# Kernel tuning notes

Hardware: AMD Instinct MI355X
Metric: run time of the kernel (lower is better)

## Reference

```python
import jax, jax.numpy as jnp
import numpy as np

N, X_DIM, Y_DIM, HID = 1024, 256, 256, 256  # HID = hidden_size // 2


def setup_inputs() -> dict:
    key = jax.random.key(0)
    ks = jax.random.split(key, 11)
    s_in = 1.0 / np.sqrt(X_DIM)
    s_h = 1.0 / np.sqrt(HID)
    return {
        "x_samples": jax.random.normal(ks[0], (N, X_DIM), jnp.float32),
        "y_samples": jax.random.normal(ks[1], (N, Y_DIM), jnp.float32),
        "z_samples": jax.random.normal(ks[2], (N, Y_DIM), jnp.float32),
        "w1_mu": jax.random.uniform(ks[3], (HID, X_DIM), jnp.float32, -s_in, s_in),
        "b1_mu": jax.random.uniform(ks[4], (HID,), jnp.float32, -s_in, s_in),
        "w2_mu": jax.random.uniform(ks[5], (Y_DIM, HID), jnp.float32, -s_h, s_h),
        "b2_mu": jax.random.uniform(ks[6], (Y_DIM,), jnp.float32, -s_h, s_h),
        "w1_lv": jax.random.uniform(ks[7], (HID, X_DIM), jnp.float32, -s_in, s_in),
        "b1_lv": jax.random.uniform(ks[8], (HID,), jnp.float32, -s_in, s_in),
        "w2_lv": jax.random.uniform(ks[9], (Y_DIM, HID), jnp.float32, -s_h, s_h),
        "b2_lv": jax.random.uniform(ks[10], (Y_DIM,), jnp.float32, -s_h, s_h),
    }


def reference(x_samples, y_samples, z_samples,
              w1_mu, b1_mu, w2_mu, b2_mu,
              w1_lv, b1_lv, w2_lv, b2_lv):
    # MLP heads (torch Linear: x @ W.T + b)
    h_mu = jax.nn.relu(x_samples @ w1_mu.T + b1_mu)
    mu = h_mu @ w2_mu.T + b2_mu                       # [N, D]
    h_lv = jax.nn.relu(x_samples @ w1_lv.T + b1_lv)
    logvar = jnp.tanh(h_lv @ w2_lv.T + b2_lv)          # [N, D]

    inv2var = 1.0 / (2.0 * jnp.exp(logvar))           # [N, D]

    # positive: per-sample conditional log-density term
    positive = -((mu - y_samples) ** 2 + (mu - z_samples) ** 2) * inv2var  # [N, D]

    # negative: mean over all pairings (i: prediction, j: sample)
    # pairwise squared diffs materialize [N, N, D] like the original broadcast
    pred = mu[:, None, :]                              # [N, 1, D]
    sq = (y_samples[None, :, :] - pred) ** 2 + (z_samples[None, :, :] - pred) ** 2
    negative = -sq.mean(axis=1) * inv2var              # [N, D]

    return jax.nn.relu(positive.sum(axis=-1) - negative.sum(axis=-1)).mean()
```

## Files before the change

### kernel.cpp

```cpp
#include <hip/hip_runtime.h>
#include <math.h>

constexpr int LSB = 72;

typedef short bf16x8 __attribute__((ext_vector_type(8)));
typedef float f32x4  __attribute__((ext_vector_type(4)));

__device__ __forceinline__ unsigned short f2bf_rne(float f) {
    unsigned u = __float_as_uint(f);
    unsigned r = (u + 0x7fff + ((u >> 16) & 1)) >> 16;
    return (unsigned short)r;
}
__device__ __forceinline__ float bf2f(unsigned short h) {
    return __uint_as_float(((unsigned)h) << 16);
}
__device__ __forceinline__ void split4(float4 v, ushort4& hi, ushort4& lo) {
    hi.x = f2bf_rne(v.x); lo.x = f2bf_rne(v.x - bf2f(hi.x));
    hi.y = f2bf_rne(v.y); lo.y = f2bf_rne(v.y - bf2f(hi.y));
    hi.z = f2bf_rne(v.z); lo.z = f2bf_rne(v.z - bf2f(hi.z));
    hi.w = f2bf_rne(v.w); lo.w = f2bf_rne(v.w - bf2f(hi.w));
}

__global__ __launch_bounds__(256, 2)
void k1_layer1(const float* __restrict__ x,
               const float* __restrict__ w1m, const float* __restrict__ w1l,
               const float* __restrict__ b1m, const float* __restrict__ b1l,
               const float* __restrict__ w2m, const float* __restrict__ w2l,
               unsigned short* __restrict__ hmH, unsigned short* __restrict__ hmL,
               unsigned short* __restrict__ hlH, unsigned short* __restrict__ hlL,
               unsigned short* __restrict__ w2mH, unsigned short* __restrict__ w2mL,
               unsigned short* __restrict__ w2lH, unsigned short* __restrict__ w2lL,
               const float* __restrict__ y, const float* __restrict__ z,
               float* __restrict__ pA1, float* __restrict__ pB1,
               float* __restrict__ rowAcc) {
    const int bid = blockIdx.x, t = threadIdx.x;
    const int head = bid & 1, ct = (bid >> 1) & 7, rt = bid >> 4;
    const int rowBase = rt * 32, colBase = ct * 32;
    const int w = t >> 6, lane = t & 63, quad = lane >> 4, mr = lane & 15;
    const int mt = w & 1, nt = w >> 1;

    const float* Bw   = head ? w1l : w1m;
    const float* bias = head ? b1l : b1m;
    unsigned short* CH = head ? hlH : hmH;
    unsigned short* CL = head ? hlL : hmL;

    __shared__ __align__(16) unsigned short Ah[32][LSB], Al[32][LSB];
    __shared__ __align__(16) unsigned short Bh[32][LSB], Bl[32][LSB];

    f32x4 acc = {0.f, 0.f, 0.f, 0.f};

    for (int kt = 0; kt < 256; kt += 64) {
#pragma unroll
        for (int p = 0; p < 2; p++) {
            int idx = p * 256 + t;
            int r = idx >> 4, k4 = idx & 15;
            float4 av = *(const float4*)&x[(rowBase + r) * 256 + kt + k4 * 4];
            float4 bv = *(const float4*)&Bw[(colBase + r) * 256 + kt + k4 * 4];
            ushort4 h4, l4;
            split4(av, h4, l4);
            *(ushort4*)&Ah[r][k4 * 4] = h4;
            *(ushort4*)&Al[r][k4 * 4] = l4;
            split4(bv, h4, l4);
            *(ushort4*)&Bh[r][k4 * 4] = h4;
            *(ushort4*)&Bl[r][k4 * 4] = l4;
        }
        __syncthreads();

#pragma unroll
        for (int kk = 0; kk < 64; kk += 32) {
            int ko = kk + quad * 8;
            bf16x8 ah = *(const bf16x8*)&Ah[mt * 16 + mr][ko];
            bf16x8 al = *(const bf16x8*)&Al[mt * 16 + mr][ko];
            bf16x8 bh = *(const bf16x8*)&Bh[nt * 16 + mr][ko];
            bf16x8 bl = *(const bf16x8*)&Bl[nt * 16 + mr][ko];
            acc = __builtin_amdgcn_mfma_f32_16x16x32_bf16(ah, bh, acc, 0, 0, 0);
            acc = __builtin_amdgcn_mfma_f32_16x16x32_bf16(ah, bl, acc, 0, 0, 0);
            acc = __builtin_amdgcn_mfma_f32_16x16x32_bf16(al, bh, acc, 0, 0, 0);
        }
        __syncthreads();
    }

    {
        int cg = colBase + nt * 16 + mr;
        float bb = bias[cg];
#pragma unroll
        for (int reg = 0; reg < 4; reg++) {
            int rg = rowBase + mt * 16 + quad * 4 + reg;
            float v = fmaxf(acc[reg] + bb, 0.f);
            unsigned short hi = f2bf_rne(v);
            CH[rg * 256 + cg] = hi;
            CL[rg * 256 + cg] = f2bf_rne(v - bf2f(hi));
        }
    }

    if (bid < 256) {
        int off = bid * 256 + t;
        float vm = w2m[off], vl = w2l[off];
        unsigned short h1 = f2bf_rne(vm);
        w2mH[off] = h1; w2mL[off] = f2bf_rne(vm - bf2f(h1));
        unsigned short h2 = f2bf_rne(vl);
        w2lH[off] = h2; w2lL[off] = f2bf_rne(vl - bf2f(h2));
    }

    if (bid < 256) {
        float sA = 0.f, sB = 0.f;
        int base = bid * 4 * 256 + t;
#pragma unroll
        for (int j = 0; j < 4; j++) {
            float yv = y[base + j * 256];
            float zv = z[base + j * 256];
            sA += yv * yv + zv * zv;
            sB += yv + zv;
        }
        pA1[bid * 256 + t] = sA;
        pB1[bid * 256 + t] = sB;
    }

    if (bid < 4) rowAcc[bid * 256 + t] = 0.f;
}

__global__ __launch_bounds__(256, 2)
void k2_fused(const unsigned short* __restrict__ hmH, const unsigned short* __restrict__ hmL,
              const unsigned short* __restrict__ hlH, const unsigned short* __restrict__ hlL,
              const unsigned short* __restrict__ w2mH, const unsigned short* __restrict__ w2mL,
              const unsigned short* __restrict__ w2lH, const unsigned short* __restrict__ w2lL,
              const float* __restrict__ b2m, const float* __restrict__ b2l,
              const float* __restrict__ y, const float* __restrict__ z,
              const float* __restrict__ pA1, const float* __restrict__ pB1,
              float* __restrict__ rowAcc) {
    const int bid = blockIdx.x, t = threadIdx.x;
    const int rt = bid >> 4, ct = bid & 15;
    const int rowBase = rt * 32, colBase = ct * 16;
    const int w = t >> 6, lane = t & 63, quad = lane >> 4, mr = lane & 15;
    const int h = w & 1, mt = w >> 1;

    __shared__ __align__(16) unsigned short Ast[2][2][32][LSB];
    __shared__ __align__(16) unsigned short Bst[2][2][16][LSB];
    __shared__ float Cx[2][32][17];
    __shared__ float part[16][16];
    __shared__ float mAf[16], mBf[16];

    const unsigned short* Aarr[4] = {hmH, hmL, hlH, hlL};
    const unsigned short* Barr[4] = {w2mH, w2mL, w2lH, w2lL};

    {
        int c = t & 15, g = t >> 4;
        int gc = colBase + c;
        float sA = 0.f, sB = 0.f;
        for (int j = 0; j < 16; j++) {
            int s = g * 16 + j;
            sA += pA1[s * 256 + gc];
        }
        part[g][c] = sA;
    }
    __syncthreads();
    if (t < 16) {
        float sA = 0.f;
#pragma unroll
        for (int g = 0; g < 16; g++) sA += part[g][t];
        mAf[t] = sA * (1.f / 1024.f);
    }
    __syncthreads();
    {
        int c = t & 15, g = t >> 4;
        int gc = colBase + c;
        float sB = 0.f;
        for (int j = 0; j < 16; j++) {
            int s = g * 16 + j;
            sB += pB1[s * 256 + gc];
        }
        part[g][c] = sB;
    }
    __syncthreads();
    if (t < 16) {
        float sB = 0.f;
#pragma unroll
        for (int g = 0; g < 16; g++) sB += part[g][t];
        mBf[t] = sB * (1.f / 1024.f);
    }

    f32x4 acc = {0.f, 0.f, 0.f, 0.f};

    for (int kt = 0; kt < 256; kt += 64) {
#pragma unroll
        for (int hp = 0; hp < 4; hp++) {
#pragma unroll
            for (int p = 0; p < 2; p++) {
                int idx = p * 256 + t;
                int r = idx >> 4, k4 = idx & 15;
                *(ushort4*)&Ast[hp >> 1][hp & 1][r][k4 * 4] =
                    *(const ushort4*)&Aarr[hp][(rowBase + r) * 256 + kt + k4 * 4];
            }
            {
                int r = t >> 4, k4 = t & 15;
                *(ushort4*)&Bst[hp >> 1][hp & 1][r][k4 * 4] =
                    *(const ushort4*)&Barr[hp][(colBase + r) * 256 + kt + k4 * 4];
            }
        }
        __syncthreads();

#pragma unroll
        for (int kk = 0; kk < 64; kk += 32) {
            int ko = kk + quad * 8;
            bf16x8 ah = *(const bf16x8*)&Ast[h][0][mt * 16 + mr][ko];
            bf16x8 al = *(const bf16x8*)&Ast[h][1][mt * 16 + mr][ko];
            bf16x8 bh = *(const bf16x8*)&Bst[h][0][mr][ko];
            bf16x8 bl = *(const bf16x8*)&Bst[h][1][mr][ko];
            acc = __builtin_amdgcn_mfma_f32_16x16x32_bf16(ah, bh, acc, 0, 0, 0);
            acc = __builtin_amdgcn_mfma_f32_16x16x32_bf16(ah, bl, acc, 0, 0, 0);
            acc = __builtin_amdgcn_mfma_f32_16x16x32_bf16(al, bh, acc, 0, 0, 0);
        }
        __syncthreads();
    }

    {
        const float* bias = h ? b2l : b2m;
        float bb = bias[colBase + mr];
#pragma unroll
        for (int reg = 0; reg < 4; reg++)
            Cx[h][mt * 16 + quad * 4 + reg][mr] = acc[reg] + bb;
    }
    __syncthreads();

    {
        int col = t & 15, rg = t >> 4;
        int gcol = colBase + col;
        float mA = mAf[col], mB = mBf[col];
#pragma unroll
        for (int rr = 0; rr < 2; rr++) {
            int row = rg * 2 + rr;
            int o = (rowBase + row) * 256 + gcol;
            float m  = Cx[0][row][col];
            float lv = tanhf(Cx[1][row][col]);
            float iv = 0.5f * expf(-lv);
            float yv = y[o];
            float zv = z[o];
            float Mt = mA - 2.f * m * mB + 2.f * m * m;
            float dy = m - yv, dz = m - zv;
            float term = iv * (Mt - dy * dy - dz * dz);
#pragma unroll
            for (int msk = 8; msk; msk >>= 1)
                term += __shfl_xor(term, msk, 16);
            if (col == 0) atomicAdd(&rowAcc[rowBase + row], term);
        }
    }
}

__global__ __launch_bounds__(256)
void k3_final(const float* __restrict__ rowAcc, float* __restrict__ out) {
    __shared__ float red[4];
    int t = threadIdx.x, lane = t & 63, wave = t >> 6;
    float v = 0.f;
#pragma unroll
    for (int p = 0; p < 4; p++)
        v += fmaxf(rowAcc[p * 256 + t], 0.f);
#pragma unroll
    for (int msk = 32; msk; msk >>= 1)
        v += __shfl_xor(v, msk, 64);
    if (lane == 0) red[wave] = v;
    __syncthreads();
    if (t == 0)
        out[0] = (red[0] + red[1] + red[2] + red[3]) * (1.f / 1024.f);
}

extern "C" void kernel_launch(void* const* d_in, const int* in_sizes, int n_in,
                              void* d_out, int out_size, void* d_ws, size_t ws_size,
                              hipStream_t stream) {
    const float* x   = (const float*)d_in[0];
    const float* y   = (const float*)d_in[1];
    const float* zs  = (const float*)d_in[2];
    const float* w1m = (const float*)d_in[3];
    const float* b1m = (const float*)d_in[4];
    const float* w2m = (const float*)d_in[5];
    const float* b2m = (const float*)d_in[6];
    const float* w1l = (const float*)d_in[7];
    const float* b1l = (const float*)d_in[8];
    const float* w2l = (const float*)d_in[9];
    const float* b2l = (const float*)d_in[10];
    float* out = (float*)d_out;

    char* ws = (char*)d_ws;
    float* pA1    = (float*)(ws);
    float* pB1    = (float*)(ws + (256u << 10));
    float* rowAcc = (float*)(ws + (512u << 10));
    unsigned short* hmH = (unsigned short*)(ws + (1024u << 10));
    unsigned short* hmL = (unsigned short*)(ws + (1536u << 10));
    unsigned short* hlH = (unsigned short*)(ws + (2048u << 10));
    unsigned short* hlL = (unsigned short*)(ws + (2560u << 10));
    unsigned short* w2mH = (unsigned short*)(ws + (3072u << 10));
    unsigned short* w2mL = (unsigned short*)(ws + (3200u << 10));
    unsigned short* w2lH = (unsigned short*)(ws + (3328u << 10));
    unsigned short* w2lL = (unsigned short*)(ws + (3456u << 10));

    k1_layer1<<<512, 256, 0, stream>>>(x, w1m, w1l, b1m, b1l, w2m, w2l,
                                       hmH, hmL, hlH, hlL,
                                       w2mH, w2mL, w2lH, w2lL,
                                       y, zs, pA1, pB1, rowAcc);
    k2_fused<<<512, 256, 0, stream>>>(hmH, hmL, hlH, hlL,
                                      w2mH, w2mL, w2lH, w2lL,
                                      b2m, b2l, y, zs, pA1, pB1, rowAcc);
    k3_final<<<1, 256, 0, stream>>>(rowAcc, out);
}
```

Measured before the change: 91.45 us.

## Split K across waves and double grid size in both GEMM kernels

Both GEMM kernels now use smaller output tiles (16 columns in layer 1, 16 rows in layer 2) with the K dimension split across wave pairs and partial sums reduced through shared memory, doubling block counts to 1040 and 1024. The y/z column-sum precompute moves to 16 dedicated blocks, each of which loops over 64 rows, and launch bounds rise to 4 blocks per CU. The aim is more parallelism and occupancy on a small problem, paid for with extra shared-memory reduction, more syncs, and redundant staging of x across more blocks.

```diff
diff --git a/kernel.cpp b/kernel.cpp
--- a/kernel.cpp
+++ b/kernel.cpp
@@ -21,7 +21,7 @@
     hi.w = f2bf_rne(v.w); lo.w = f2bf_rne(v.w - bf2f(hi.w));
 }
 
-__global__ __launch_bounds__(256, 2)
+__global__ __launch_bounds__(256, 4)
 void k1_layer1(const float* __restrict__ x,
                const float* __restrict__ w1m, const float* __restrict__ w1l,
                const float* __restrict__ b1m, const float* __restrict__ b1l,
@@ -34,45 +34,68 @@
                float* __restrict__ pA1, float* __restrict__ pB1,
                float* __restrict__ rowAcc) {
     const int bid = blockIdx.x, t = threadIdx.x;
-    const int head = bid & 1, ct = (bid >> 1) & 7, rt = bid >> 4;
-    const int rowBase = rt * 32, colBase = ct * 32;
+
+    if (bid < 16) {
+        float sA = 0.f, sB = 0.f;
+        int base = bid * 64 * 256 + t;
+        for (int j = 0; j < 64; j++) {
+            float yv = y[base + j * 256];
+            float zv = z[base + j * 256];
+            sA += yv * yv + zv * zv;
+            sB += yv + zv;
+        }
+        pA1[bid * 256 + t] = sA;
+        pB1[bid * 256 + t] = sB;
+        return;
+    }
+
+    const int g = bid - 16;
+    const int head = g & 1, ct = (g >> 1) & 15, rt = g >> 5;
+    const int rowBase = rt * 32, colBase = ct * 16;
     const int w = t >> 6, lane = t & 63, quad = lane >> 4, mr = lane & 15;
-    const int mt = w & 1, nt = w >> 1;
+    const int mt = w & 1, ks = w >> 1;
 
     const float* Bw   = head ? w1l : w1m;
     const float* bias = head ? b1l : b1m;
     unsigned short* CH = head ? hlH : hmH;
     unsigned short* CL = head ? hlL : hmL;
 
-    __shared__ __align__(16) unsigned short Ah[32][LSB], Al[32][LSB];
-    __shared__ __align__(16) unsigned short Bh[32][LSB], Bl[32][LSB];
+    __shared__ __align__(16) unsigned short Ast[2][2][32][LSB];
+    __shared__ __align__(16) unsigned short Bst[2][2][16][LSB];
+    __shared__ float Cx[2][16][17];
 
     f32x4 acc = {0.f, 0.f, 0.f, 0.f};
 
-    for (int kt = 0; kt < 256; kt += 64) {
+    for (int sub = 0; sub < 2; sub++) {
+#pragma unroll
+        for (int p = 0; p < 4; p++) {
+            int idx = p * 256 + t;
+            int q = idx >> 9, r = (idx >> 4) & 31, k4 = idx & 15;
+            float4 av = *(const float4*)&x[(rowBase + r) * 256 + q * 128 + sub * 64 + k4 * 4];
+            ushort4 h4, l4;
+            split4(av, h4, l4);
+            *(ushort4*)&Ast[q][0][r][k4 * 4] = h4;
+            *(ushort4*)&Ast[q][1][r][k4 * 4] = l4;
+        }
 #pragma unroll
         for (int p = 0; p < 2; p++) {
             int idx = p * 256 + t;
-            int r = idx >> 4, k4 = idx & 15;
-            float4 av = *(const float4*)&x[(rowBase + r) * 256 + kt + k4 * 4];
-            float4 bv = *(const float4*)&Bw[(colBase + r) * 256 + kt + k4 * 4];
+            int q = idx >> 8, r = (idx >> 4) & 15, k4 = idx & 15;
+            float4 bv = *(const float4*)&Bw[(colBase + r) * 256 + q * 128 + sub * 64 + k4 * 4];
             ushort4 h4, l4;
-            split4(av, h4, l4);
-            *(ushort4*)&Ah[r][k4 * 4] = h4;
-            *(ushort4*)&Al[r][k4 * 4] = l4;
             split4(bv, h4, l4);
-            *(ushort4*)&Bh[r][k4 * 4] = h4;
-            *(ushort4*)&Bl[r][k4 * 4] = l4;
+            *(ushort4*)&Bst[q][0][r][k4 * 4] = h4;
+            *(ushort4*)&Bst[q][1][r][k4 * 4] = l4;
         }
         __syncthreads();
 
 #pragma unroll
         for (int kk = 0; kk < 64; kk += 32) {
             int ko = kk + quad * 8;
-            bf16x8 ah = *(const bf16x8*)&Ah[mt * 16 + mr][ko];
-            bf16x8 al = *(const bf16x8*)&Al[mt * 16 + mr][ko];
-            bf16x8 bh = *(const bf16x8*)&Bh[nt * 16 + mr][ko];
-            bf16x8 bl = *(const bf16x8*)&Bl[nt * 16 + mr][ko];
+            bf16x8 ah = *(const bf16x8*)&Ast[ks][0][mt * 16 + mr][ko];
+            bf16x8 al = *(const bf16x8*)&Ast[ks][1][mt * 16 + mr][ko];
+            bf16x8 bh = *(const bf16x8*)&Bst[ks][0][mr][ko];
+            bf16x8 bl = *(const bf16x8*)&Bst[ks][1][mr][ko];
             acc = __builtin_amdgcn_mfma_f32_16x16x32_bf16(ah, bh, acc, 0, 0, 0);
             acc = __builtin_amdgcn_mfma_f32_16x16x32_bf16(ah, bl, acc, 0, 0, 0);
             acc = __builtin_amdgcn_mfma_f32_16x16x32_bf16(al, bh, acc, 0, 0, 0);
@@ -80,21 +103,27 @@
         __syncthreads();
     }
 
-    {
-        int cg = colBase + nt * 16 + mr;
+    if (ks == 1) {
+#pragma unroll
+        for (int reg = 0; reg < 4; reg++)
+            Cx[mt][quad * 4 + reg][mr] = acc[reg];
+    }
+    __syncthreads();
+    if (ks == 0) {
+        int cg = colBase + mr;
         float bb = bias[cg];
 #pragma unroll
         for (int reg = 0; reg < 4; reg++) {
             int rg = rowBase + mt * 16 + quad * 4 + reg;
-            float v = fmaxf(acc[reg] + bb, 0.f);
+            float v = fmaxf(acc[reg] + Cx[mt][quad * 4 + reg][mr] + bb, 0.f);
             unsigned short hi = f2bf_rne(v);
             CH[rg * 256 + cg] = hi;
             CL[rg * 256 + cg] = f2bf_rne(v - bf2f(hi));
         }
     }
 
-    if (bid < 256) {
-        int off = bid * 256 + t;
+    if (g < 256) {
+        int off = g * 256 + t;
         float vm = w2m[off], vl = w2l[off];
         unsigned short h1 = f2bf_rne(vm);
         w2mH[off] = h1; w2mL[off] = f2bf_rne(vm - bf2f(h1));
@@ -102,24 +131,10 @@
         w2lH[off] = h2; w2lL[off] = f2bf_rne(vl - bf2f(h2));
     }
 
-    if (bid < 256) {
-        float sA = 0.f, sB = 0.f;
-        int base = bid * 4 * 256 + t;
-#pragma unroll
-        for (int j = 0; j < 4; j++) {
-            float yv = y[base + j * 256];
-            float zv = z[base + j * 256];
-            sA += yv * yv + zv * zv;
-            sB += yv + zv;
-        }
-        pA1[bid * 256 + t] = sA;
-        pB1[bid * 256 + t] = sB;
-    }
-
-    if (bid < 4) rowAcc[bid * 256 + t] = 0.f;
-}
-
-__global__ __launch_bounds__(256, 2)
+    if (g < 4) rowAcc[g * 256 + t] = 0.f;
+}
+
+__global__ __launch_bounds__(256, 4)
 void k2_fused(const unsigned short* __restrict__ hmH, const unsigned short* __restrict__ hmL,
               const unsigned short* __restrict__ hlH, const unsigned short* __restrict__ hlL,
               const unsigned short* __restrict__ w2mH, const unsigned short* __restrict__ w2mL,
@@ -130,82 +145,58 @@
               float* __restrict__ rowAcc) {
     const int bid = blockIdx.x, t = threadIdx.x;
     const int rt = bid >> 4, ct = bid & 15;
-    const int rowBase = rt * 32, colBase = ct * 16;
+    const int rowBase = rt * 16, colBase = ct * 16;
     const int w = t >> 6, lane = t & 63, quad = lane >> 4, mr = lane & 15;
-    const int h = w & 1, mt = w >> 1;
-
-    __shared__ __align__(16) unsigned short Ast[2][2][32][LSB];
-    __shared__ __align__(16) unsigned short Bst[2][2][16][LSB];
-    __shared__ float Cx[2][32][17];
-    __shared__ float part[16][16];
-    __shared__ float mAf[16], mBf[16];
+    const int h = w & 1, ks = w >> 1;
+
+    __shared__ __align__(16) char smem[39232];
+    auto Ast = (unsigned short (*)[4][16][LSB])(smem);
+    auto Bst = (unsigned short (*)[4][16][LSB])(smem + 18432);
+    auto CxP = (float (*)[16][17])(smem + 36864);
+    float* mAf = (float*)(smem + 39040);
+    float* mBf = (float*)(smem + 39104);
+    float (*partA)[16] = (float (*)[16])(smem);
+    float (*partB)[16] = (float (*)[16])(smem + 1024);
 
     const unsigned short* Aarr[4] = {hmH, hmL, hlH, hlL};
     const unsigned short* Barr[4] = {w2mH, w2mL, w2lH, w2lL};
 
     {
-        int c = t & 15, g = t >> 4;
-        int gc = colBase + c;
+        int s = t >> 4, c = t & 15;
+        partA[s][c] = pA1[s * 256 + colBase + c];
+        partB[s][c] = pB1[s * 256 + colBase + c];
+    }
+    __syncthreads();
+    if (t < 16) {
         float sA = 0.f, sB = 0.f;
-        for (int j = 0; j < 16; j++) {
-            int s = g * 16 + j;
-            sA += pA1[s * 256 + gc];
-        }
-        part[g][c] = sA;
-    }
-    __syncthreads();
-    if (t < 16) {
-        float sA = 0.f;
-#pragma unroll
-        for (int g = 0; g < 16; g++) sA += part[g][t];
+#pragma unroll
+        for (int s = 0; s < 16; s++) { sA += partA[s][t]; sB += partB[s][t]; }
         mAf[t] = sA * (1.f / 1024.f);
-    }
-    __syncthreads();
-    {
-        int c = t & 15, g = t >> 4;
-        int gc = colBase + c;
-        float sB = 0.f;
-        for (int j = 0; j < 16; j++) {
-            int s = g * 16 + j;
-            sB += pB1[s * 256 + gc];
-        }
-        part[g][c] = sB;
-    }
-    __syncthreads();
-    if (t < 16) {
-        float sB = 0.f;
-#pragma unroll
-        for (int g = 0; g < 16; g++) sB += part[g][t];
         mBf[t] = sB * (1.f / 1024.f);
     }
+    __syncthreads();
 
     f32x4 acc = {0.f, 0.f, 0.f, 0.f};
 
-    for (int kt = 0; kt < 256; kt += 64) {
-#pragma unroll
-        for (int hp = 0; hp < 4; hp++) {
-#pragma unroll
-            for (int p = 0; p < 2; p++) {
-                int idx = p * 256 + t;
-                int r = idx >> 4, k4 = idx & 15;
-                *(ushort4*)&Ast[hp >> 1][hp & 1][r][k4 * 4] =
-                    *(const ushort4*)&Aarr[hp][(rowBase + r) * 256 + kt + k4 * 4];
-            }
-            {
-                int r = t >> 4, k4 = t & 15;
-                *(ushort4*)&Bst[hp >> 1][hp & 1][r][k4 * 4] =
-                    *(const ushort4*)&Barr[hp][(colBase + r) * 256 + kt + k4 * 4];
-            }
+    for (int sub = 0; sub < 2; sub++) {
+#pragma unroll
+        for (int p = 0; p < 8; p++) {
+            int idx = p * 256 + t;
+            int hp = idx >> 9, q = (idx >> 8) & 1, r = (idx >> 4) & 15, k4 = idx & 15;
+            *(ushort4*)&Ast[q][hp][r][k4 * 4] =
+                *(const ushort4*)&Aarr[hp][(rowBase + r) * 256 + q * 128 + sub * 64 + k4 * 4];
+            *(ushort4*)&Bst[q][hp][r][k4 * 4] =
+                *(const ushort4*)&Barr[hp][(colBase + r) * 256 + q * 128 + sub * 64 + k4 * 4];
         }
         __syncthreads();
 
 #pragma unroll
         for (int kk = 0; kk < 64; kk += 32) {
             int ko = kk + quad * 8;
-            bf16x8 ah = *(const bf16x8*)&Ast[h][0][mt * 16 + mr][ko];
-            bf16x8 al = *(const bf16x8*)&Ast[h][1][mt * 16 + mr][ko];
-            bf16x8 bh = *(const bf16x8*)&Bst[h][0][mr][ko];
-            bf16x8 bl = *(const bf16x8*)&Bst[h][1][mr][ko];
+            bf16x8 ah = *(const bf16x8*)&Ast[ks][h * 2 + 0][mr][ko];
+            bf16x8 al = *(const bf16x8*)&Ast[ks][h * 2 + 1][mr][ko];
+            bf16x8 bh = *(const bf16x8*)&Bst[ks][h * 2 + 0][mr][ko];
+            bf16x8 bl = *(const bf16x8*)&Bst[ks][h * 2 + 1][mr][ko];
             acc = __builtin_amdgcn_mfma_f32_16x16x32_bf16(ah, bh, acc, 0, 0, 0);
             acc = __builtin_amdgcn_mfma_f32_16x16x32_bf16(ah, bl, acc, 0, 0, 0);
             acc = __builtin_amdgcn_mfma_f32_16x16x32_bf16(al, bh, acc, 0, 0, 0);
@@ -213,36 +204,35 @@
         __syncthreads();
     }
 
+    if (ks == 1) {
+#pragma unroll
+        for (int reg = 0; reg < 4; reg++)
+            CxP[h][quad * 4 + reg][mr] = acc[reg];
+    }
+    __syncthreads();
+    if (ks == 0) {
+        float bb = (h ? b2l : b2m)[colBase + mr];
+#pragma unroll
+        for (int reg = 0; reg < 4; reg++)
+            CxP[h][quad * 4 + reg][mr] += acc[reg] + bb;
+    }
+    __syncthreads();
+
     {
-        const float* bias = h ? b2l : b2m;
-        float bb = bias[colBase + mr];
-#pragma unroll
-        for (int reg = 0; reg < 4; reg++)
-            Cx[h][mt * 16 + quad * 4 + reg][mr] = acc[reg] + bb;
-    }
-    __syncthreads();
-
-    {
-        int col = t & 15, rg = t >> 4;
-        int gcol = colBase + col;
-        float mA = mAf[col], mB = mBf[col];
-#pragma unroll
-        for (int rr = 0; rr < 2; rr++) {
-            int row = rg * 2 + rr;
-            int o = (rowBase + row) * 256 + gcol;
-            float m  = Cx[0][row][col];
-            float lv = tanhf(Cx[1][row][col]);
-            float iv = 0.5f * expf(-lv);
-            float yv = y[o];
-            float zv = z[o];
-            float Mt = mA - 2.f * m * mB + 2.f * m * m;
-            float dy = m - yv, dz = m - zv;
-            float term = iv * (Mt - dy * dy - dz * dz);
-#pragma unroll
-            for (int msk = 8; msk; msk >>= 1)
-                term += __shfl_xor(term, msk, 16);
-            if (col == 0) atomicAdd(&rowAcc[rowBase + row], term);
-        }
+        int row = t >> 4, col = t & 15;
+        int o = (rowBase + row) * 256 + colBase + col;
+        float m  = CxP[0][row][col];
+        float lv = tanhf(CxP[1][row][col]);
+        float iv = 0.5f * expf(-lv);
+        float yv = y[o];
+        float zv = z[o];
+        float Mt = mAf[col] - 2.f * m * mBf[col] + 2.f * m * m;
+        float dy = m - yv, dz = m - zv;
+        float term = iv * (Mt - dy * dy - dz * dz);
+#pragma unroll
+        for (int msk = 8; msk; msk >>= 1)
+            term += __shfl_xor(term, msk, 16);
+        if (col == 0) atomicAdd(&rowAcc[rowBase + row], term);
     }
 }
 
@@ -292,12 +282,12 @@
     unsigned short* w2lH = (unsigned short*)(ws + (3328u << 10));
     unsigned short* w2lL = (unsigned short*)(ws + (3456u << 10));
 
-    k1_layer1<<<512, 256, 0, stream>>>(x, w1m, w1l, b1m, b1l, w2m, w2l,
-                                       hmH, hmL, hlH, hlL,
+    k1_layer1<<<1040, 256, 0, stream>>>(x, w1m, w1l, b1m, b1l, w2m, w2l,
+                                        hmH, hmL, hlH, hlL,
+                                        w2mH, w2mL, w2lH, w2lL,
+                                        y, zs, pA1, pB1, rowAcc);
+    k2_fused<<<1024, 256, 0, stream>>>(hmH, hmL, hlH, hlL,
                                        w2mH, w2mL, w2lH, w2lL,
-                                       y, zs, pA1, pB1, rowAcc);
-    k2_fused<<<512, 256, 0, stream>>>(hmH, hmL, hlH, hlL,
-                                      w2mH, w2mL, w2lH, w2lL,
-                                      b2m, b2l, y, zs, pA1, pB1, rowAcc);
+                                       b2m, b2l, y, zs, pA1, pB1, rowAcc);
     k3_final<<<1, 256, 0, stream>>>(rowAcc, out);
 }
```

New measurement: 94.15 us. +2.9%, slower.
